# Kernel tuning notes

Measured on AMD Instinct MI355X. Metric: run time of the kernel, lower is better.

## Reference

```python
import jax, jax.numpy as jnp
import numpy as np

B, C, T = 8, 512, 4096
KC, VC, H = 512, 512, 1  # key_channels, value_channels, num_heads
SCALE = KC // (H ** 0.5)  # faithful to original: key_channels // num_heads**0.5


def setup_inputs() -> dict:
    key = jax.random.key(0)
    k1, k2, k3, k4, k5 = jax.random.split(key, 5)
    x = jax.random.normal(k1, (B, C, T), dtype=jnp.float32)
    # 1x1 Conv1d weights: Conv1d(C, out, kernel_size=1) == per-timestep Linear
    Wqk = jax.random.normal(k2, (KC, C), dtype=jnp.float32) / np.sqrt(C)
    bqk = jax.random.normal(k3, (KC,), dtype=jnp.float32) * 0.01
    Wv = jax.random.normal(k4, (VC, C), dtype=jnp.float32) / np.sqrt(C)
    bv = jax.random.normal(k5, (VC,), dtype=jnp.float32) * 0.01
    return {"x": x, "Wqk": Wqk, "bqk": bqk, "Wv": Wv, "bv": bv}


def reference(x, Wqk, bqk, Wv, bv):
    # 1x1 conv projections: [B,C,T] -> [B,K,T] / [B,V,T]
    qk = jnp.einsum('kc,bct->bkt', Wqk, x) + bqk[None, :, None]
    val = jnp.einsum('vc,bct->bvt', Wv, x) + bv[None, :, None]
    # channel-wise attention: with num_heads=1 the reshape/transpose/matmul
    # chain reduces to scores[b,k,v] = sum_t qk[b,k,t] * val[b,v,t]
    scores = jnp.einsum('bkt,bvt->bkv', qk, val) / SCALE
    p = jax.nn.softmax(scores, axis=-1)          # softmax over value channels
    # inference path: dropout is identity (self.training == False)
    out = jnp.einsum('bkv,bvt->bkt', p, val)     # [B,K,T], K == input_channels
    return out.reshape(-1, C, T)
```

## Files before the change

### kernel.cpp

```cpp
#include <hip/hip_runtime.h>
#include <hip/hip_bf16.h>


#define BB 8
#define CC 512
#define TT 4096

typedef __attribute__((ext_vector_type(8))) short bf16x8;
typedef __attribute__((ext_vector_type(4))) float f32x4;

__device__ __forceinline__ void gload_lds16(const void* g, void* l) {
  __builtin_amdgcn_global_load_lds((const __attribute__((address_space(1))) void*)g,
                                   (__attribute__((address_space(3))) void*)l,
                                   16, 0, 0);
}
__device__ __forceinline__ float bf2f(short u) {
  return __uint_as_float(((unsigned)(unsigned short)u) << 16);
}
__device__ __forceinline__ unsigned short f2bf(float f) {
  return __builtin_bit_cast(unsigned short, __float2bfloat16(f));
}

__global__ __launch_bounds__(256)
void convert_x_kernel(const float* __restrict__ x, __hip_bfloat16* __restrict__ xh,
                      __hip_bfloat16* __restrict__ xhT, float* __restrict__ sx)
{
  __shared__ float tile[32][33];
  const int b = blockIdx.z, c0 = blockIdx.y * 32, t0 = blockIdx.x * 32;
  const int tid = threadIdx.x;
  {
    const int c = tid >> 3, t4 = (tid & 7) * 4;
    const size_t gi = ((size_t)b * CC + (c0 + c)) * TT + t0 + t4;
    const float4 v = *(const float4*)&x[gi];
    ushort4 h;
    h.x = f2bf(v.x); h.y = f2bf(v.y); h.z = f2bf(v.z); h.w = f2bf(v.w);
    *(ushort4*)&xh[gi] = h;
    tile[c][t4 + 0] = v.x; tile[c][t4 + 1] = v.y;
    tile[c][t4 + 2] = v.z; tile[c][t4 + 3] = v.w;
    float s = (v.x + v.y) + (v.z + v.w);
    s += __shfl_xor(s, 1); s += __shfl_xor(s, 2); s += __shfl_xor(s, 4);
    if ((tid & 7) == 0) atomicAdd(&sx[b * CC + c0 + c], s);
  }
  __syncthreads();
  {
    const int t = tid >> 3, c4 = (tid & 7) * 4;
    ushort4 h;
    h.x = f2bf(tile[c4 + 0][t]); h.y = f2bf(tile[c4 + 1][t]);
    h.z = f2bf(tile[c4 + 2][t]); h.w = f2bf(tile[c4 + 3][t]);
    *(ushort4*)&xhT[((size_t)b * TT + (t0 + t)) * CC + c0 + c4] = h;
  }
}

__global__ __launch_bounds__(256)
void convert_w_kernel(const float* __restrict__ Wqk, const float* __restrict__ Wv,
                      __hip_bfloat16* __restrict__ Wqkh, __hip_bfloat16* __restrict__ Wvh,
                      __hip_bfloat16* __restrict__ WvT)
{
  int i = blockIdx.x * 256 + threadIdx.x;
  Wqkh[i] = __float2bfloat16(Wqk[i]);
  float wv = Wv[i];
  Wvh[i] = __float2bfloat16(wv);
  WvT[(i & 511) * 512 + (i >> 9)] = __float2bfloat16(wv);
}

__global__ __launch_bounds__(256)
void tatb_kernel(const float* __restrict__ Wqk, const float* __restrict__ Wv,
                 const float* __restrict__ sx, float* __restrict__ ta, float* __restrict__ tb)
{
  int wid = threadIdx.x >> 6, lane = threadIdx.x & 63;
  int gid = blockIdx.x * 4 + wid;
  int which = gid >> 12;
  int rem = gid & 4095;
  int b = rem >> 9, j = rem & 511;
  const float* W = which ? Wv : Wqk;
  float s = 0.f;
#pragma unroll
  for (int i = 0; i < 8; i++) {
    int c = lane + i * 64;
    s += W[j * 512 + c] * sx[b * 512 + c];
  }
#pragma unroll
  for (int off = 32; off; off >>= 1) s += __shfl_xor(s, off);
  if (lane == 0) (which ? tb : ta)[b * 512 + j] = s;
}

template <int BM, int BN, int EPI>
__global__ __launch_bounds__(256)
void gemm_nt_kernel(const __hip_bfloat16* __restrict__ A, long strideA, int ldA,
                    const __hip_bfloat16* __restrict__ B, long strideB, int ldB,
                    void* __restrict__ C, long strideC, int ldC,
                    int Kslice, int nslices,
                    const float* __restrict__ p1, const float* __restrict__ p2,
                    const float* __restrict__ p3, const float* __restrict__ p4)
{
  constexpr int FM = BM / 32, FN = BN / 32;
  const int tid = threadIdx.x, lane = tid & 63, wid = tid >> 6;

  const int gx = gridDim.x, gy = gridDim.y;
  const int lin = blockIdx.x + gx * (blockIdx.y + gy * blockIdx.z);
  const int nwg = gx * gy * (int)gridDim.z;
  const int lin2 = (lin & 7) * (nwg >> 3) + (lin >> 3);
  const int tn = lin2 % gx;
  const int r1 = lin2 / gx;
  const int tm = r1 % gy;
  const int z  = r1 / gy;
  const int b  = z / nslices;
  const int ks = z - b * nslices;

  const __hip_bfloat16* Ab = A + (size_t)b * strideA + (size_t)(tm * BM) * ldA + (size_t)ks * Kslice;
  const __hip_bfloat16* Bb = B + (size_t)b * strideB + (size_t)(tn * BN) * ldB + (size_t)ks * Kslice;

  __shared__ __align__(16) __hip_bfloat16 sA[BM * 64];
  __shared__ __align__(16) __hip_bfloat16 sB[BN * 64];

  const int wr = wid >> 1, wc = wid & 1;

  f32x4 acc[FM][FN];
#pragma unroll
  for (int m = 0; m < FM; m++)
#pragma unroll
    for (int n = 0; n < FN; n++) acc[m][n] = (f32x4){0.f, 0.f, 0.f, 0.f};

  for (int k0 = 0; k0 < Kslice; k0 += 64) {
#pragma unroll
    for (int i = 0; i < BM / 32; i++) {
      int e = tid * 8 + i * 2048;
      int row = e >> 6;
      int colg = (e & 63) ^ ((row & 7) << 3);
      gload_lds16(Ab + (size_t)row * ldA + k0 + colg, &sA[wid * 512 + i * 2048]);
    }
#pragma unroll
    for (int i = 0; i < BN / 32; i++) {
      int e = tid * 8 + i * 2048;
      int row = e >> 6;
      int colg = (e & 63) ^ ((row & 7) << 3);
      gload_lds16(Bb + (size_t)row * ldB + k0 + colg, &sB[wid * 512 + i * 2048]);
    }
    __syncthreads();
#pragma unroll
    for (int ks2 = 0; ks2 < 2; ks2++) {
      bf16x8 af[FM], bfv[FN];
      const int kb = ks2 * 32 + (lane >> 4) * 8;
#pragma unroll
      for (int m = 0; m < FM; m++) {
        int row = wr * (BM / 2) + m * 16 + (lane & 15);
        af[m] = *(const bf16x8*)&sA[row * 64 + (kb ^ ((row & 7) << 3))];
      }
#pragma unroll
      for (int n = 0; n < FN; n++) {
        int row = wc * (BN / 2) + n * 16 + (lane & 15);
        bfv[n] = *(const bf16x8*)&sB[row * 64 + (kb ^ ((row & 7) << 3))];
      }
#pragma unroll
      for (int m = 0; m < FM; m++)
#pragma unroll
        for (int n = 0; n < FN; n++)
          acc[m][n] = __builtin_amdgcn_mfma_f32_16x16x32_bf16(af[m], bfv[n], acc[m][n], 0, 0, 0);
    }
    __syncthreads();
  }

  const int rb = tm * BM + wr * (BM / 2) + ((lane >> 4) << 2);
  const int cb = tn * BN + wc * (BN / 2) + (lane & 15);

  if (EPI == 0) {
    __hip_bfloat16* Cb = (__hip_bfloat16*)C + (size_t)z * strideC;
#pragma unroll
    for (int m = 0; m < FM; m++)
#pragma unroll
      for (int n = 0; n < FN; n++)
#pragma unroll
        for (int r = 0; r < 4; r++) {
          int row = rb + m * 16 + r, col = cb + n * 16;
          Cb[(size_t)row * ldC + col] = __float2bfloat16(acc[m][n][r]);
        }
  } else if (EPI == 1) {
    float* Cf = (float*)C + (size_t)z * strideC;
    const float* ta = p3 + b * 512;
    const float* tb = p4 + b * 512;
#pragma unroll
    for (int m = 0; m < FM; m++)
#pragma unroll
      for (int n = 0; n < FN; n++)
#pragma unroll
        for (int r = 0; r < 4; r++) {
          int row = rb + m * 16 + r, col = cb + n * 16;
          float bq = p1[row], bvv = p2[col];
          float v = acc[m][n][r] + bq * tb[col] + bvv * ta[row] + (float)TT * bq * bvv;
          Cf[(size_t)row * ldC + col] = v * (1.0f / 512.0f);
        }
  } else {
    float* Cf = (float*)C + (size_t)z * strideC;
    const float* pb = p1 + b * 512;
#pragma unroll
    for (int m = 0; m < FM; m++)
#pragma unroll
      for (int n = 0; n < FN; n++)
#pragma unroll
        for (int r = 0; r < 4; r++) {
          int row = rb + m * 16 + r, col = cb + n * 16;
          Cf[(size_t)row * ldC + col] = acc[m][n][r] + pb[row];
        }
  }
}

__global__ __launch_bounds__(256)
void reduce_g_kernel(const short* __restrict__ Gpart, short* __restrict__ Gb)
{
  const int idx = (blockIdx.x * 256 + threadIdx.x) * 8;
  const int b = idx >> 18, i = idx & 262143;
  const short* base = Gpart + ((size_t)(b * 4) << 18) + i;
  float s[8];
#pragma unroll
  for (int q = 0; q < 8; q++) s[q] = 0.f;
#pragma unroll
  for (int ks = 0; ks < 4; ks++) {
    bf16x8 v = *(const bf16x8*)(base + ((size_t)ks << 18));
#pragma unroll
    for (int q = 0; q < 8; q++) s[q] += bf2f(v[q]);
  }
  bf16x8 o;
#pragma unroll
  for (int q = 0; q < 8; q++) o[q] = (short)f2bf(s[q]);
  *(bf16x8*)(Gb + ((size_t)b << 18) + i) = o;
}

__global__ __launch_bounds__(256)
void softmax_kernel(const float* __restrict__ scores, const float* __restrict__ bv,
                    __hip_bfloat16* __restrict__ p, float* __restrict__ pb)
{
  const int row = blockIdx.x;
  const int tid = threadIdx.x;
  const float s0 = scores[(size_t)row * 512 + tid];
  const float s1 = scores[(size_t)row * 512 + 256 + tid];
  __shared__ float red[4];

  float m = fmaxf(s0, s1);
#pragma unroll
  for (int off = 32; off; off >>= 1) m = fmaxf(m, __shfl_xor(m, off));
  if ((tid & 63) == 0) red[tid >> 6] = m;
  __syncthreads();
  m = fmaxf(fmaxf(red[0], red[1]), fmaxf(red[2], red[3]));

  float e0 = __expf(s0 - m), e1 = __expf(s1 - m);
  float s = e0 + e1;
#pragma unroll
  for (int off = 32; off; off >>= 1) s += __shfl_xor(s, off);
  __syncthreads();
  if ((tid & 63) == 0) red[tid >> 6] = s;
  __syncthreads();
  s = red[0] + red[1] + red[2] + red[3];
  float inv = 1.0f / s;

  float p0 = e0 * inv, p1v = e1 * inv;
  p[(size_t)row * 512 + tid] = __float2bfloat16(p0);
  p[(size_t)row * 512 + 256 + tid] = __float2bfloat16(p1v);

  float contrib = p0 * bv[tid] + p1v * bv[256 + tid];
#pragma unroll
  for (int off = 32; off; off >>= 1) contrib += __shfl_xor(contrib, off);
  __syncthreads();
  if ((tid & 63) == 0) red[tid >> 6] = contrib;
  __syncthreads();
  if (tid == 0) pb[row] = red[0] + red[1] + red[2] + red[3];
}

extern "C" void kernel_launch(void* const* d_in, const int* in_sizes, int n_in,
                              void* d_out, int out_size, void* d_ws, size_t ws_size,
                              hipStream_t stream)
{
  const float* x   = (const float*)d_in[0];
  const float* Wqk = (const float*)d_in[1];
  const float* bqk = (const float*)d_in[2];
  const float* Wv  = (const float*)d_in[3];
  const float* bv  = (const float*)d_in[4];
  float* out = (float*)d_out;

  char* w = (char*)d_ws;
  auto alloc = [&](size_t bytes) {
    void* pp = (void*)w;
    w += (bytes + 255) & ~(size_t)255;
    return pp;
  };
  __hip_bfloat16* xh     = (__hip_bfloat16*)alloc((size_t)BB * CC * TT * 2);
  __hip_bfloat16* xhT    = (__hip_bfloat16*)alloc((size_t)BB * TT * CC * 2);
  short*          Gpart  = (short*)alloc((size_t)BB * 4 * CC * CC * 2);
  short*          Gb     = (short*)alloc((size_t)BB * CC * CC * 2);
  __hip_bfloat16* S2     = (__hip_bfloat16*)alloc((size_t)BB * CC * CC * 2);
  float*          scores = (float*)alloc((size_t)BB * CC * CC * 4);
  __hip_bfloat16* pmat   = (__hip_bfloat16*)alloc((size_t)BB * CC * CC * 2);
  __hip_bfloat16* Mm     = (__hip_bfloat16*)alloc((size_t)BB * CC * CC * 2);
  __hip_bfloat16* Wqkh   = (__hip_bfloat16*)alloc((size_t)CC * CC * 2);
  __hip_bfloat16* Wvh    = (__hip_bfloat16*)alloc((size_t)CC * CC * 2);
  __hip_bfloat16* WvT    = (__hip_bfloat16*)alloc((size_t)CC * CC * 2);
  float* sx = (float*)alloc((size_t)BB * CC * 4);
  float* ta = (float*)alloc((size_t)BB * CC * 4);
  float* tb = (float*)alloc((size_t)BB * CC * 4);
  float* pb = (float*)alloc((size_t)BB * CC * 4);

  hipMemsetAsync(sx, 0, (size_t)BB * CC * 4, stream);

  convert_x_kernel<<<dim3(TT / 32, CC / 32, BB), 256, 0, stream>>>(x, xh, xhT, sx);
  convert_w_kernel<<<(CC * CC) / 256, 256, 0, stream>>>(Wqk, Wv, Wqkh, Wvh, WvT);
  tatb_kernel<<<(2 * BB * CC) / 4, 256, 0, stream>>>(Wqk, Wv, sx, ta, tb);

  const long sXH = (long)CC * TT;
  const long sSq = (long)CC * CC;

  gemm_nt_kernel<128, 128, 0><<<dim3(4, 4, BB * 4), 256, 0, stream>>>(
      xh, sXH, TT, xh, sXH, TT, Gpart, sSq, CC, 1024, 4,
      nullptr, nullptr, nullptr, nullptr);
  reduce_g_kernel<<<(BB * CC * CC) / (256 * 8), 256, 0, stream>>>(Gpart, Gb);

  gemm_nt_kernel<64, 64, 0><<<dim3(8, 8, BB), 256, 0, stream>>>(
      Wvh, 0, CC, (const __hip_bfloat16*)Gb, sSq, CC, S2, sSq, CC, 512, 1,
      nullptr, nullptr, nullptr, nullptr);

  gemm_nt_kernel<64, 64, 1><<<dim3(8, 8, BB), 256, 0, stream>>>(
      Wqkh, 0, CC, S2, sSq, CC, scores, sSq, CC, 512, 1,
      bqk, bv, ta, tb);

  softmax_kernel<<<BB * CC, 256, 0, stream>>>(scores, bv, pmat, pb);

  gemm_nt_kernel<64, 64, 0><<<dim3(8, 8, BB), 256, 0, stream>>>(
      pmat, sSq, CC, WvT, 0, CC, Mm, sSq, CC, 512, 1,
      nullptr, nullptr, nullptr, nullptr);

  gemm_nt_kernel<128, 128, 2><<<dim3(TT / 128, 4, BB), 256, 0, stream>>>(
      Mm, sSq, CC, xhT, (long)TT * CC, CC, out, (long)CC * TT, TT, 512, 1,
      pb, nullptr, nullptr, nullptr);
}
```

Baseline: 237.5 us.

## Drop transposed x copy; use LDS transpose reads and double-buffered GEMMs

The x conversion kernel becomes a flat streaming bf16 cast plus row sums, so the transposed bf16 copy of x is no longer written. A new output GEMM reads the untransposed xh and uses ds_read_b64_tr_b16 LDS transpose loads to build the B operand. The generic GEMM also gets double-buffered LDS so the next K tile loads while the current one computes. The goal is to cut about 32MB of transposed writes and the strided shared-memory transpose, at the cost of doubled LDS use (lower occupancy) and hand-written inline asm waits.

```diff
diff --git a/kernel.cpp b/kernel.cpp
--- a/kernel.cpp
+++ b/kernel.cpp
@@ -7,6 +7,7 @@
 #define TT 4096
 
 typedef __attribute__((ext_vector_type(8))) short bf16x8;
+typedef __attribute__((ext_vector_type(4))) short bf16x4;
 typedef __attribute__((ext_vector_type(4))) float f32x4;
 
 __device__ __forceinline__ void gload_lds16(const void* g, void* l) {
@@ -22,32 +23,26 @@
 }
 
 __global__ __launch_bounds__(256)
-void convert_x_kernel(const float* __restrict__ x, __hip_bfloat16* __restrict__ xh,
-                      __hip_bfloat16* __restrict__ xhT, float* __restrict__ sx)
-{
-  __shared__ float tile[32][33];
-  const int b = blockIdx.z, c0 = blockIdx.y * 32, t0 = blockIdx.x * 32;
-  const int tid = threadIdx.x;
-  {
-    const int c = tid >> 3, t4 = (tid & 7) * 4;
-    const size_t gi = ((size_t)b * CC + (c0 + c)) * TT + t0 + t4;
-    const float4 v = *(const float4*)&x[gi];
-    ushort4 h;
-    h.x = f2bf(v.x); h.y = f2bf(v.y); h.z = f2bf(v.z); h.w = f2bf(v.w);
-    *(ushort4*)&xh[gi] = h;
-    tile[c][t4 + 0] = v.x; tile[c][t4 + 1] = v.y;
-    tile[c][t4 + 2] = v.z; tile[c][t4 + 3] = v.w;
-    float s = (v.x + v.y) + (v.z + v.w);
-    s += __shfl_xor(s, 1); s += __shfl_xor(s, 2); s += __shfl_xor(s, 4);
-    if ((tid & 7) == 0) atomicAdd(&sx[b * CC + c0 + c], s);
-  }
-  __syncthreads();
-  {
-    const int t = tid >> 3, c4 = (tid & 7) * 4;
-    ushort4 h;
-    h.x = f2bf(tile[c4 + 0][t]); h.y = f2bf(tile[c4 + 1][t]);
-    h.z = f2bf(tile[c4 + 2][t]); h.w = f2bf(tile[c4 + 3][t]);
-    *(ushort4*)&xhT[((size_t)b * TT + (t0 + t)) * CC + c0 + c4] = h;
+void convert_stream_kernel(const float* __restrict__ x, __hip_bfloat16* __restrict__ xh,
+                           float* __restrict__ sx)
+{
+  const int gid = blockIdx.x * 256 + threadIdx.x;
+#pragma unroll
+  for (int it = 0; it < 4; it++) {
+    const int chunk = it * 524288 + gid;
+    const size_t base = (size_t)chunk * 8;
+    const float4 a = *(const float4*)&x[base];
+    const float4 c = *(const float4*)&x[base + 4];
+    bf16x8 h;
+    h[0] = (short)f2bf(a.x); h[1] = (short)f2bf(a.y);
+    h[2] = (short)f2bf(a.z); h[3] = (short)f2bf(a.w);
+    h[4] = (short)f2bf(c.x); h[5] = (short)f2bf(c.y);
+    h[6] = (short)f2bf(c.z); h[7] = (short)f2bf(c.w);
+    *(bf16x8*)&xh[base] = h;
+    float s = ((a.x + a.y) + (a.z + a.w)) + ((c.x + c.y) + (c.z + c.w));
+#pragma unroll
+    for (int off = 32; off; off >>= 1) s += __shfl_xor(s, off);
+    if ((threadIdx.x & 63) == 0) atomicAdd(&sx[chunk >> 9], s);
   }
 }
 
@@ -110,8 +105,8 @@
   const __hip_bfloat16* Ab = A + (size_t)b * strideA + (size_t)(tm * BM) * ldA + (size_t)ks * Kslice;
   const __hip_bfloat16* Bb = B + (size_t)b * strideB + (size_t)(tn * BN) * ldB + (size_t)ks * Kslice;
 
-  __shared__ __align__(16) __hip_bfloat16 sA[BM * 64];
-  __shared__ __align__(16) __hip_bfloat16 sB[BN * 64];
+  __shared__ __align__(16) __hip_bfloat16 sA[2][BM * 64];
+  __shared__ __align__(16) __hip_bfloat16 sB[2][BN * 64];
 
   const int wr = wid >> 1, wc = wid & 1;
 
@@ -121,22 +116,28 @@
 #pragma unroll
     for (int n = 0; n < FN; n++) acc[m][n] = (f32x4){0.f, 0.f, 0.f, 0.f};
 
-  for (int k0 = 0; k0 < Kslice; k0 += 64) {
+  auto stage = [&](int buf, int k0) {
 #pragma unroll
     for (int i = 0; i < BM / 32; i++) {
       int e = tid * 8 + i * 2048;
-      int row = e >> 6;
-      int colg = (e & 63) ^ ((row & 7) << 3);
-      gload_lds16(Ab + (size_t)row * ldA + k0 + colg, &sA[wid * 512 + i * 2048]);
+      int row = e >> 6, colg = (e & 63) ^ ((row & 7) << 3);
+      gload_lds16(Ab + (size_t)row * ldA + k0 + colg, &sA[buf][wid * 512 + i * 2048]);
     }
 #pragma unroll
     for (int i = 0; i < BN / 32; i++) {
       int e = tid * 8 + i * 2048;
-      int row = e >> 6;
-      int colg = (e & 63) ^ ((row & 7) << 3);
-      gload_lds16(Bb + (size_t)row * ldB + k0 + colg, &sB[wid * 512 + i * 2048]);
+      int row = e >> 6, colg = (e & 63) ^ ((row & 7) << 3);
+      gload_lds16(Bb + (size_t)row * ldB + k0 + colg, &sB[buf][wid * 512 + i * 2048]);
     }
-    __syncthreads();
+  };
+
+  stage(0, 0);
+  __syncthreads();
+  const int nsteps = Kslice >> 6;
+  for (int s = 0; s < nsteps; s++) {
+    if (s + 1 < nsteps) stage((s + 1) & 1, (s + 1) << 6);
+    const __hip_bfloat16* cA = sA[s & 1];
+    const __hip_bfloat16* cB = sB[s & 1];
 #pragma unroll
     for (int ks2 = 0; ks2 < 2; ks2++) {
       bf16x8 af[FM], bfv[FN];
@@ -144,12 +145,12 @@
 #pragma unroll
       for (int m = 0; m < FM; m++) {
         int row = wr * (BM / 2) + m * 16 + (lane & 15);
-        af[m] = *(const bf16x8*)&sA[row * 64 + (kb ^ ((row & 7) << 3))];
+        af[m] = *(const bf16x8*)&cA[row * 64 + (kb ^ ((row & 7) << 3))];
       }
 #pragma unroll
       for (int n = 0; n < FN; n++) {
         int row = wc * (BN / 2) + n * 16 + (lane & 15);
-        bfv[n] = *(const bf16x8*)&sB[row * 64 + (kb ^ ((row & 7) << 3))];
+        bfv[n] = *(const bf16x8*)&cB[row * 64 + (kb ^ ((row & 7) << 3))];
       }
 #pragma unroll
       for (int m = 0; m < FM; m++)
@@ -265,6 +266,113 @@
   if (tid == 0) pb[row] = red[0] + red[1] + red[2] + red[3];
 }
 
+__global__ __launch_bounds__(256)
+void gemm_out_kernel(const __hip_bfloat16* __restrict__ Mall,
+                     const __hip_bfloat16* __restrict__ xh,
+                     const float* __restrict__ pball,
+                     float* __restrict__ out)
+{
+  __shared__ __align__(16) __hip_bfloat16 sA[2][128 * 64];
+  __shared__ __align__(16) __hip_bfloat16 sB[2][64 * 128];
+
+  const int tid = threadIdx.x, lane = tid & 63, wid = tid >> 6;
+  const int wr = wid >> 1, wc = wid & 1;
+
+  const int lin = blockIdx.x + 32 * (blockIdx.y + 4 * blockIdx.z);
+  const int lin2 = (lin & 7) * 128 + (lin >> 3);
+  const int tn = lin2 & 31;
+  const int tm = (lin2 >> 5) & 3;
+  const int b  = lin2 >> 7;
+
+  const __hip_bfloat16* Ab = Mall + (size_t)b * 262144 + (size_t)(tm * 128) * 512;
+  const __hip_bfloat16* Bb = xh + (size_t)b * ((size_t)CC * TT) + tn * 128;
+
+  f32x4 acc[4][4];
+#pragma unroll
+  for (int m = 0; m < 4; m++)
+#pragma unroll
+    for (int n = 0; n < 4; n++) acc[m][n] = (f32x4){0.f, 0.f, 0.f, 0.f};
+
+  auto stage = [&](int buf, int k0) {
+#pragma unroll
+    for (int i = 0; i < 4; i++) {
+      int e = tid * 8 + i * 2048;
+      int row = e >> 6, colg = (e & 63) ^ ((row & 7) << 3);
+      gload_lds16(Ab + (size_t)row * 512 + k0 + colg, &sA[buf][wid * 512 + i * 2048]);
+    }
+#pragma unroll
+    for (int q = 0; q < 4; q++) {
+      int E = q * 2048 + tid * 8;
+      int v = ((E >> 9) << 2) | ((E >> 4) & 3);
+      int t = (((E >> 6) & 7) << 4) | (E & 8);
+      gload_lds16(Bb + (size_t)(k0 + v) * TT + t, &sB[buf][wid * 512 + q * 2048]);
+    }
+  };
+
+  const unsigned sB32 =
+      (unsigned)(size_t)(__attribute__((address_space(3))) __hip_bfloat16*)&sB[0][0];
+  const unsigned btr_lo = sB32 + (lane >> 4) * 2048 + (lane & 15) * 8 + wc * 512;
+  const unsigned btr_hi = btr_lo + 8192;
+
+#define COMPUTE(BUF)                                                            \
+  {                                                                             \
+    _Pragma("unroll")                                                           \
+    for (int ks2 = 0; ks2 < 2; ks2++) {                                         \
+      bf16x8 af[4]; bf16x4 blo[4], bhi[4];                                      \
+      const int kb = ks2 * 32 + (lane >> 4) * 8;                                \
+      _Pragma("unroll")                                                         \
+      for (int m = 0; m < 4; m++) {                                             \
+        int row = wr * 64 + m * 16 + (lane & 15);                               \
+        af[m] = *(const bf16x8*)&sA[BUF][row * 64 + (kb ^ ((row & 7) << 3))];   \
+      }                                                                         \
+      unsigned ab = ks2 ? btr_hi : btr_lo;                                      \
+      _Pragma("unroll")                                                         \
+      for (int n = 0; n < 4; n++) {                                             \
+        asm volatile("ds_read_b64_tr_b16 %0, %1 offset:%2"                      \
+                     : "=v"(blo[n]) : "v"(ab), "i"((BUF) * 16384 + n * 128));   \
+        asm volatile("ds_read_b64_tr_b16 %0, %1 offset:%2"                      \
+                     : "=v"(bhi[n]) : "v"(ab), "i"((BUF) * 16384 + n * 128 + 1024)); \
+      }                                                                         \
+      asm volatile("s_waitcnt lgkmcnt(0)" ::: "memory");                        \
+      __builtin_amdgcn_sched_barrier(0);                                        \
+      _Pragma("unroll")                                                         \
+      for (int m = 0; m < 4; m++)                                               \
+        _Pragma("unroll")                                                       \
+        for (int n = 0; n < 4; n++) {                                           \
+          bf16x8 b8 = __builtin_shufflevector(blo[n], bhi[n], 0, 1, 2, 3, 4, 5, 6, 7); \
+          acc[m][n] = __builtin_amdgcn_mfma_f32_16x16x32_bf16(af[m], b8, acc[m][n], 0, 0, 0); \
+        }                                                                       \
+    }                                                                           \
+  }
+
+  stage(0, 0);
+  __syncthreads();
+#pragma unroll 1
+  for (int s = 0; s < 8; s += 2) {
+    if (s + 1 < 8) stage(1, (s + 1) * 64);
+    COMPUTE(0);
+    __syncthreads();
+    if (s + 2 < 8) stage(0, (s + 2) * 64);
+    COMPUTE(1);
+    __syncthreads();
+  }
+#undef COMPUTE
+
+  const int rb = tm * 128 + wr * 64 + ((lane >> 4) << 2);
+  const int cb = tn * 128 + wc * 64 + (lane & 15);
+  float* Cf = out + (size_t)b * ((size_t)CC * TT);
+  const float* pb = pball + b * 512;
+#pragma unroll
+  for (int m = 0; m < 4; m++)
+#pragma unroll
+    for (int n = 0; n < 4; n++)
+#pragma unroll
+      for (int r = 0; r < 4; r++) {
+        int row = rb + m * 16 + r, col = cb + n * 16;
+        Cf[(size_t)row * TT + col] = acc[m][n][r] + pb[row];
+      }
+}
+
 extern "C" void kernel_launch(void* const* d_in, const int* in_sizes, int n_in,
                               void* d_out, int out_size, void* d_ws, size_t ws_size,
                               hipStream_t stream)
@@ -283,7 +391,6 @@
     return pp;
   };
   __hip_bfloat16* xh     = (__hip_bfloat16*)alloc((size_t)BB * CC * TT * 2);
-  __hip_bfloat16* xhT    = (__hip_bfloat16*)alloc((size_t)BB * TT * CC * 2);
   short*          Gpart  = (short*)alloc((size_t)BB * 4 * CC * CC * 2);
   short*          Gb     = (short*)alloc((size_t)BB * CC * CC * 2);
   __hip_bfloat16* S2     = (__hip_bfloat16*)alloc((size_t)BB * CC * CC * 2);
@@ -300,7 +407,7 @@
 
   hipMemsetAsync(sx, 0, (size_t)BB * CC * 4, stream);
 
-  convert_x_kernel<<<dim3(TT / 32, CC / 32, BB), 256, 0, stream>>>(x, xh, xhT, sx);
+  convert_stream_kernel<<<2048, 256, 0, stream>>>(x, xh, sx);
   convert_w_kernel<<<(CC * CC) / 256, 256, 0, stream>>>(Wqk, Wv, Wqkh, Wvh, WvT);
   tatb_kernel<<<(2 * BB * CC) / 4, 256, 0, stream>>>(Wqk, Wv, sx, ta, tb);
 
@@ -326,7 +433,5 @@
       pmat, sSq, CC, WvT, 0, CC, Mm, sSq, CC, 512, 1,
       nullptr, nullptr, nullptr, nullptr);
 
-  gemm_nt_kernel<128, 128, 2><<<dim3(TT / 128, 4, BB), 256, 0, stream>>>(
-      Mm, sSq, CC, xhT, (long)TT * CC, CC, out, (long)CC * TT, TT, 512, 1,
-      pb, nullptr, nullptr, nullptr);
-}
+  gemm_out_kernel<<<dim3(32, 4, 8), 256, 0, stream>>>(Mm, xh, pb, out);
+}
```

After: 214.2 us. -9.8%, faster.
